# Kernel tuning notes

Hardware: AMD Instinct MI355X
Metric: run time of the kernel (lower is better)

Reference implementation:

```python
import jax, jax.numpy as jnp
import numpy as np

B, N, D, OUT = 4, 4096, 2048, 2048
E, RANK, TOP_K = 8, 16, 2
ALPHA = 16.0
SCALING = ALPHA / RANK


def setup_inputs() -> dict:
    key = jax.random.key(0)
    k1, k2, k3, k4 = jax.random.split(key, 4)
    x = jax.random.normal(k1, (B, N, D), dtype=jnp.float32)
    weight = jax.random.normal(k2, (OUT, D), dtype=jnp.float32) * (1.0 / np.sqrt(D))
    router_w = jax.random.normal(k3, (E, D), dtype=jnp.float32) * 0.02
    experts_A = jax.random.normal(k4, (E, D, RANK), dtype=jnp.float32) * (1.0 / np.sqrt(RANK))
    # experts_B is zero-initialized in the module; use small random values so the
    # LoRA branch contributes non-trivially to the output for kernel testing.
    experts_B = jax.random.normal(jax.random.fold_in(key, 5), (E, RANK, OUT), dtype=jnp.float32) * 0.02
    return {"x": x, "weight": weight, "router_w": router_w,
            "experts_A": experts_A, "experts_B": experts_B}


def reference(x, weight, router_w, experts_A, experts_B):
    # base = F.linear(x, weight)  (no bias)
    base = jnp.einsum('bnd,od->bno', x, weight)
    # router logits: x @ W_r^T -> (B, N, E)
    logits = jnp.einsum('bnd,ed->bne', x, router_w)
    # top-k sparse routing: keep top-k logits, set rest to -inf, softmax
    topk_vals, topk_idx = jax.lax.top_k(logits, TOP_K)  # (B,N,K)
    keep = jax.nn.one_hot(topk_idx, E, dtype=jnp.bool_).any(axis=-2)  # (B,N,E)
    masked = jnp.where(keep, logits, -jnp.inf)
    router_weights = jax.nn.softmax(masked, axis=-1)  # (B,N,E)
    # per-expert low-rank down/up projection, weighted by router
    lora_down = jnp.einsum('bnd,edr->bner', x, experts_A)  # (B,N,E,rank)
    weighted = lora_down * router_weights[..., None]
    moe_out = jnp.einsum('bner,erd->bnd', weighted, experts_B)  # (B,N,OUT)
    return base + SCALING * moe_out
```

## Files before the change

kernel.cpp:

```cpp
#include <hip/hip_runtime.h>
#include <stdint.h>

#define D_DIM 2048
#define OUT_DIM 2048
#define NTOK 16384
#define SCALING 1.0f
#define NT_TILES 34

typedef unsigned short u16;
typedef __attribute__((ext_vector_type(8))) short s16x8;
typedef __attribute__((ext_vector_type(4))) float f32x4;

#define WZ_OFF  0u
#define AZ_OFF  8388608u
#define BZ_OFF  8912896u
#define CZ_OFF  9437184u
#define W8_OFF  13631488u
#define XB_OFF  14155776u
#define WS_BIG   81264640u

__device__ inline u16 f2bf(float f) {
  union { float f; uint32_t u; } v; v.f = f;
  uint32_t u = v.u;
  u += 0x7FFFu + ((u >> 16) & 1u);
  return (u16)(u >> 16);
}

__global__ __launch_bounds__(256) void k_prep(const float* __restrict__ W,
                                              const float* __restrict__ A,
                                              const float* __restrict__ Bf,
                                              u16* __restrict__ Wz,
                                              u16* __restrict__ Az,
                                              u16* __restrict__ Bz) {
  int bid = blockIdx.x;
  if (bid < 4096) {
    int idx = bid * 256 + threadIdx.x;
    int o  = idx >> 9;
    int k0 = (idx & 511) * 4;
    const float4 v = *(const float4*)&W[(size_t)o * D_DIM + k0];
    int s = (o & 7) << 3;
    int dst = (k0 & ~63) | ((k0 & 63) ^ s);
    uint32_t p0 = (uint32_t)f2bf(v.x) | ((uint32_t)f2bf(v.y) << 16);
    uint32_t p1 = (uint32_t)f2bf(v.z) | ((uint32_t)f2bf(v.w) << 16);
    *(uint2*)&Wz[(size_t)o * D_DIM + dst] = make_uint2(p0, p1);
  } else if (bid < 5120) {
    int idx = (bid - 4096) * 256 + threadIdx.x;
    float v = A[idx];
    int r = idx & 15;
    int d = (idx >> 4) & 2047;
    int e = idx >> 15;
    int er = e * 16 + r;
    int s = (er & 7) << 3;
    int dst = (d & ~63) | ((d & 63) ^ s);
    Az[(size_t)er * D_DIM + dst] = f2bf(v);
  } else {
    int idx = (bid - 5120) * 256 + threadIdx.x;
    float v = Bf[idx];
    int er = idx >> 11;
    int o  = idx & 2047;
    int s = (o & 7) << 3;
    int dst = (er & 64) | ((er & 63) ^ s);
    Bz[(size_t)o * 128 + dst] = f2bf(v);
  }
}

__global__ __launch_bounds__(256) void k_router_xb(const float* __restrict__ x,
                                                   const float* __restrict__ rw,
                                                   float* __restrict__ w8,
                                                   u16* __restrict__ xb) {
  int lane = threadIdx.x & 63, wid = threadIdx.x >> 6;
  int t = blockIdx.x * 4 + wid;
  const float* xr = x + (size_t)t * D_DIM;
  float4 xv[8];
#pragma unroll
  for (int j = 0; j < 8; ++j) xv[j] = *(const float4*)&xr[j * 256 + lane * 4];
  int s = (t & 7) << 3;
#pragma unroll
  for (int j = 0; j < 8; ++j) {
    int c4 = j * 256 + lane * 4;
    int dst = (c4 & ~63) | ((c4 & 63) ^ s);
    uint32_t p0 = (uint32_t)f2bf(xv[j].x) | ((uint32_t)f2bf(xv[j].y) << 16);
    uint32_t p1 = (uint32_t)f2bf(xv[j].z) | ((uint32_t)f2bf(xv[j].w) << 16);
    *(uint2*)&xb[(size_t)t * D_DIM + dst] = make_uint2(p0, p1);
  }
  float lg[8];
#pragma unroll
  for (int e = 0; e < 8; ++e) {
    float a = 0.f;
#pragma unroll
    for (int j = 0; j < 8; ++j) {
      float4 rv = *(const float4*)&rw[e * D_DIM + j * 256 + lane * 4];
      a = fmaf(xv[j].x, rv.x, a); a = fmaf(xv[j].y, rv.y, a);
      a = fmaf(xv[j].z, rv.z, a); a = fmaf(xv[j].w, rv.w, a);
    }
#pragma unroll
    for (int off = 32; off; off >>= 1) a += __shfl_xor(a, off, 64);
    lg[e] = a;
  }
  int i0 = 0;
#pragma unroll
  for (int e = 1; e < 8; ++e) if (lg[e] > lg[i0]) i0 = e;
  int i1 = (i0 == 0) ? 1 : 0;
#pragma unroll
  for (int e = 0; e < 8; ++e) if (e != i0 && lg[e] > lg[i1]) i1 = e;
  float e1 = expf(lg[i1] - lg[i0]);
  float inv = 1.f / (1.f + e1);
  float w0 = inv * SCALING, w1 = e1 * inv * SCALING;
  if (lane < 8)
    w8[(size_t)t * 8 + lane] = (lane == i0) ? w0 : (lane == i1) ? w1 : 0.f;
}

__global__ __launch_bounds__(256) void k_lora64(const u16* __restrict__ xb,
                                                const u16* __restrict__ Az,
                                                const float* __restrict__ w8,
                                                u16* __restrict__ Cz) {
  __shared__ u16 Alds[64 * 64];
  __shared__ u16 Blds[128 * 64];
  __shared__ float w8s[64 * 8];
  int tid = threadIdx.x, lane = tid & 63, wid = tid >> 6;
  int t0 = blockIdx.x * 64;
  w8s[tid] = w8[(size_t)t0 * 8 + tid];
  w8s[256 + tid] = w8[(size_t)t0 * 8 + 256 + tid];
  f32x4 acc[8];
#pragma unroll
  for (int n = 0; n < 8; ++n) acc[n] = (f32x4){0.f, 0.f, 0.f, 0.f};
  const int ce = (lane >> 4) * 8;
  for (int kc = 0; kc < 32; ++kc) {
    __syncthreads();
#pragma unroll
    for (int i = 0; i < 2; ++i) {
      const u16* g = xb + (size_t)(t0 + i * 32 + (tid >> 3)) * D_DIM + kc * 64 + (tid & 7) * 8;
      __builtin_amdgcn_global_load_lds(
          (const __attribute__((address_space(1))) void*)g,
          (__attribute__((address_space(3))) void*)(Alds + i * 2048 + tid * 8), 16, 0, 0);
    }
#pragma unroll
    for (int i = 0; i < 4; ++i) {
      const u16* g = Az + (size_t)(i * 32 + (tid >> 3)) * D_DIM + kc * 64 + (tid & 7) * 8;
      __builtin_amdgcn_global_load_lds(
          (const __attribute__((address_space(1))) void*)g,
          (__attribute__((address_space(3))) void*)(Blds + i * 2048 + tid * 8), 16, 0, 0);
    }
    __syncthreads();
#pragma unroll
    for (int kk = 0; kk < 2; ++kk) {
      int ar = wid * 16 + (lane & 15);
      s16x8 af = *(const s16x8*)&Alds[ar * 64 + ((ce + kk * 32) ^ ((ar & 7) << 3))];
#pragma unroll
      for (int nf = 0; nf < 8; ++nf) {
        int br = nf * 16 + (lane & 15);
        s16x8 bf = *(const s16x8*)&Blds[br * 64 + ((ce + kk * 32) ^ ((br & 7) << 3))];
        acc[nf] = __builtin_amdgcn_mfma_f32_16x16x32_bf16(af, bf, acc[nf], 0, 0, 0);
      }
    }
  }
#pragma unroll
  for (int q = 0; q < 4; ++q) {
    int rloc = wid * 16 + (lane >> 4) * 4 + q;
#pragma unroll
    for (int nf = 0; nf < 8; ++nf) {
      int er = nf * 16 + (lane & 15);
      float v = acc[nf][q] * w8s[rloc * 8 + (er >> 4)];
      int dst = (er & 64) | ((er & 63) ^ ((rloc & 7) << 3));
      Cz[(size_t)(t0 + rloc) * 128 + dst] = f2bf(v);
    }
  }
}

__device__ inline void stg(int kt, int h, int t0, int o0,
                           const u16* __restrict__ xb, const u16* __restrict__ Wz,
                           const u16* __restrict__ Cz, const u16* __restrict__ Bz,
                           u16* AshP, u16* BshP, int tid) {
  int p = kt & 1;
  const u16* src; int ld; size_t r0; int c0; u16* dst;
  if (h < 2) {
    if (kt < 32) { src = xb; ld = D_DIM; c0 = kt * 64; }
    else         { src = Cz; ld = 128;   c0 = (kt - 32) * 64; }
    r0 = (size_t)t0 + h * 128;
    dst = AshP + p * 16384 + h * 8192;
  } else {
    if (kt < 32) { src = Wz; ld = D_DIM; c0 = kt * 64; }
    else         { src = Bz; ld = 128;   c0 = (kt - 32) * 64; }
    r0 = (size_t)o0 + (h - 2) * 128;
    dst = BshP + p * 16384 + (h - 2) * 8192;
  }
#pragma unroll
  for (int i = 0; i < 2; ++i) {
    const u16* g = src + (r0 + i * 64 + (tid >> 3)) * (size_t)ld + c0 + (tid & 7) * 8;
    __builtin_amdgcn_global_load_lds(
        (const __attribute__((address_space(1))) void*)g,
        (__attribute__((address_space(3))) void*)(dst + i * 4096 + tid * 8), 16, 0, 0);
  }
}

__device__ inline void read_af(const u16* buf, int rbase, int ce, s16x8 a[4][2]) {
#pragma unroll
  for (int i = 0; i < 4; ++i)
#pragma unroll
    for (int kk = 0; kk < 2; ++kk) {
      int r = rbase + i * 16;
      a[i][kk] = *(const s16x8*)&buf[r * 64 + ((ce + kk * 32) ^ ((r & 7) << 3))];
    }
}

__device__ inline void read_b2(const u16* buf, int rbase, int ce, s16x8 b[4][2], int h) {
#pragma unroll
  for (int i = 0; i < 2; ++i)
#pragma unroll
    for (int kk = 0; kk < 2; ++kk) {
      int r = rbase + (h * 2 + i) * 16;
      b[h * 2 + i][kk] = *(const s16x8*)&buf[r * 64 + ((ce + kk * 32) ^ ((r & 7) << 3))];
    }
}

template <int MFH, int NFH>
__device__ inline void mfma_quad(f32x4 acc[8][4], const s16x8 a[4][2],
                                 const s16x8 b[4][2]) {
#pragma unroll
  for (int i = 0; i < 4; ++i)
#pragma unroll
    for (int j = 0; j < 2; ++j)
#pragma unroll
      for (int kk = 0; kk < 2; ++kk)
        acc[MFH * 4 + i][NFH * 2 + j] = __builtin_amdgcn_mfma_f32_16x16x32_bf16(
            a[i][kk], b[NFH * 2 + j][kk], acc[MFH * 4 + i][NFH * 2 + j], 0, 0, 0);
}

__global__ __launch_bounds__(512, 2) void k_main8(const u16* __restrict__ xb,
                                                  const u16* __restrict__ Wz,
                                                  const u16* __restrict__ Cz,
                                                  const u16* __restrict__ Bz,
                                                  float* __restrict__ out) {
  __shared__ u16 Ash[2][16384];
  __shared__ u16 Bsh[2][16384];
  const int tid = threadIdx.x, lane = tid & 63;
  const int wid = tid >> 6, wm = wid >> 2, wn = wid & 3;
  int bid = blockIdx.x;
  int swz = (bid & 7) * 64 + (bid >> 3);
  int mt = swz >> 3, nt = swz & 7;
  int t0 = mt * 256, o0 = nt * 256;
  const int ce = (lane >> 4) * 8;
  const int arb = wm * 128 + (lane & 15);
  const int brb = wn * 64 + (lane & 15);
  u16* A0 = &Ash[0][0];
  u16* B0 = &Bsh[0][0];

  f32x4 acc[8][4];
#pragma unroll
  for (int m = 0; m < 8; ++m)
#pragma unroll
    for (int n = 0; n < 4; ++n) acc[m][n] = (f32x4){0.f, 0.f, 0.f, 0.f};
  s16x8 a[4][2], b[4][2];

  stg(0, 0, t0, o0, xb, Wz, Cz, Bz, A0, B0, tid);
  stg(0, 1, t0, o0, xb, Wz, Cz, Bz, A0, B0, tid);
  stg(0, 2, t0, o0, xb, Wz, Cz, Bz, A0, B0, tid);
  stg(0, 3, t0, o0, xb, Wz, Cz, Bz, A0, B0, tid);
  stg(1, 0, t0, o0, xb, Wz, Cz, Bz, A0, B0, tid);
  stg(1, 1, t0, o0, xb, Wz, Cz, Bz, A0, B0, tid);
  stg(1, 2, t0, o0, xb, Wz, Cz, Bz, A0, B0, tid);
  stg(1, 3, t0, o0, xb, Wz, Cz, Bz, A0, B0, tid);
  asm volatile("s_waitcnt vmcnt(8)" ::: "memory");
  __builtin_amdgcn_s_barrier();

  for (int kt = 0; kt < NT_TILES; ++kt) {
    const int p = kt & 1;
    const u16* Abuf = &Ash[p][0];
    const u16* Bbuf = &Bsh[p][0];
    const int ktc = (kt + 2 < NT_TILES) ? kt + 2 : NT_TILES - 1;
    read_af(Abuf, arb, ce, a);
    read_b2(Bbuf, brb, ce, b, 0);
    __builtin_amdgcn_s_barrier();
    asm volatile("s_waitcnt lgkmcnt(0)" ::: "memory");
    __builtin_amdgcn_sched_barrier(0);
    __builtin_amdgcn_s_setprio(1);
    mfma_quad<0, 0>(acc, a, b);
    __builtin_amdgcn_s_setprio(0);
    __builtin_amdgcn_s_barrier();
    read_b2(Bbuf, brb, ce, b, 1);
    __builtin_amdgcn_s_barrier();
    asm volatile("s_waitcnt lgkmcnt(0)" ::: "memory");
    __builtin_amdgcn_sched_barrier(0);
    __builtin_amdgcn_s_setprio(1);
    mfma_quad<0, 1>(acc, a, b);
    __builtin_amdgcn_s_setprio(0);
    __builtin_amdgcn_s_barrier();
    read_af(Abuf, arb + 64, ce, a);
    stg(ktc, 2, t0, o0, xb, Wz, Cz, Bz, A0, B0, tid);
    stg(ktc, 3, t0, o0, xb, Wz, Cz, Bz, A0, B0, tid);
    __builtin_amdgcn_s_barrier();
    asm volatile("s_waitcnt lgkmcnt(0)" ::: "memory");
    __builtin_amdgcn_sched_barrier(0);
    __builtin_amdgcn_s_setprio(1);
    mfma_quad<1, 0>(acc, a, b);
    __builtin_amdgcn_s_setprio(0);
    __builtin_amdgcn_s_barrier();
    stg(ktc, 0, t0, o0, xb, Wz, Cz, Bz, A0, B0, tid);
    stg(ktc, 1, t0, o0, xb, Wz, Cz, Bz, A0, B0, tid);
    asm volatile("s_waitcnt vmcnt(8)" ::: "memory");
    __builtin_amdgcn_s_barrier();
    __builtin_amdgcn_s_setprio(1);
    mfma_quad<1, 1>(acc, a, b);
    __builtin_amdgcn_s_setprio(0);
    __builtin_amdgcn_s_barrier();
  }

#pragma unroll
  for (int mf = 0; mf < 8; ++mf)
#pragma unroll
    for (int q = 0; q < 4; ++q) {
      int row = t0 + wm * 128 + mf * 16 + (lane >> 4) * 4 + q;
#pragma unroll
      for (int nf = 0; nf < 4; ++nf) {
        int col = o0 + wn * 64 + nf * 16 + (lane & 15);
        out[(size_t)row * OUT_DIM + col] = acc[mf][nf][q];
      }
    }
}

extern "C" void kernel_launch(void* const* d_in, const int* in_sizes, int n_in,
                              void* d_out, int out_size, void* d_ws, size_t ws_size,
                              hipStream_t stream) {
  const float* x  = (const float*)d_in[0];
  const float* W  = (const float*)d_in[1];
  const float* rw = (const float*)d_in[2];
  const float* eA = (const float*)d_in[3];
  const float* eB = (const float*)d_in[4];
  float* out = (float*)d_out;
  char* ws = (char*)d_ws;
  if (ws_size < WS_BIG) return;

  u16*   Wz = (u16*)(ws + WZ_OFF);
  u16*   Az = (u16*)(ws + AZ_OFF);
  u16*   Bz = (u16*)(ws + BZ_OFF);
  u16*   Cz = (u16*)(ws + CZ_OFF);
  float* w8 = (float*)(ws + W8_OFF);
  u16*   xb = (u16*)(ws + XB_OFF);

  k_prep<<<6144, 256, 0, stream>>>(W, eA, eB, Wz, Az, Bz);
  k_router_xb<<<4096, 256, 0, stream>>>(x, rw, w8, xb);
  k_lora64<<<256, 256, 0, stream>>>(xb, Az, w8, Cz);
  k_main8<<<512, 512, 0, stream>>>(xb, Wz, Cz, Bz, out);
}
```

Measured before the change: 267.1 us.

## Fuse prep and router kernels, double-buffer LoRA loads, restructure main GEMM pipeline

Merges the weight-prep and router/x-conversion kernels into one launch, removing a kernel boundary. The LoRA down-projection kernel gains double-buffered LDS staging, so the next K-chunk loads while MFMAs run on the current one. The main GEMM loop is reorganised so that global-to-LDS stages for tile kt+1/kt+2 and LDS fragment reads for the next tile are issued earlier, with fewer barriers per iteration. This raises LDS use in k_lora64 and makes correctness depend on careful vmcnt/barrier accounting.

```diff
diff --git a/kernel.cpp b/kernel.cpp
--- a/kernel.cpp
+++ b/kernel.cpp
@@ -26,12 +26,12 @@
   return (u16)(u >> 16);
 }
 
-__global__ __launch_bounds__(256) void k_prep(const float* __restrict__ W,
-                                              const float* __restrict__ A,
-                                              const float* __restrict__ Bf,
-                                              u16* __restrict__ Wz,
-                                              u16* __restrict__ Az,
-                                              u16* __restrict__ Bz) {
+__global__ __launch_bounds__(256) void k_prep_router(
+    const float* __restrict__ W, const float* __restrict__ A,
+    const float* __restrict__ Bf, const float* __restrict__ x,
+    const float* __restrict__ rw,
+    u16* __restrict__ Wz, u16* __restrict__ Az, u16* __restrict__ Bz,
+    float* __restrict__ w8, u16* __restrict__ xb) {
   int bid = blockIdx.x;
   if (bid < 4096) {
     int idx = bid * 256 + threadIdx.x;
@@ -43,7 +43,9 @@
     uint32_t p0 = (uint32_t)f2bf(v.x) | ((uint32_t)f2bf(v.y) << 16);
     uint32_t p1 = (uint32_t)f2bf(v.z) | ((uint32_t)f2bf(v.w) << 16);
     *(uint2*)&Wz[(size_t)o * D_DIM + dst] = make_uint2(p0, p1);
-  } else if (bid < 5120) {
+    return;
+  }
+  if (bid < 5120) {
     int idx = (bid - 4096) * 256 + threadIdx.x;
     float v = A[idx];
     int r = idx & 15;
@@ -53,7 +55,9 @@
     int s = (er & 7) << 3;
     int dst = (d & ~63) | ((d & 63) ^ s);
     Az[(size_t)er * D_DIM + dst] = f2bf(v);
-  } else {
+    return;
+  }
+  if (bid < 6144) {
     int idx = (bid - 5120) * 256 + threadIdx.x;
     float v = Bf[idx];
     int er = idx >> 11;
@@ -61,15 +65,10 @@
     int s = (o & 7) << 3;
     int dst = (er & 64) | ((er & 63) ^ s);
     Bz[(size_t)o * 128 + dst] = f2bf(v);
-  }
-}
-
-__global__ __launch_bounds__(256) void k_router_xb(const float* __restrict__ x,
-                                                   const float* __restrict__ rw,
-                                                   float* __restrict__ w8,
-                                                   u16* __restrict__ xb) {
+    return;
+  }
   int lane = threadIdx.x & 63, wid = threadIdx.x >> 6;
-  int t = blockIdx.x * 4 + wid;
+  int t = (bid - 6144) * 4 + wid;
   const float* xr = x + (size_t)t * D_DIM;
   float4 xv[8];
 #pragma unroll
@@ -114,8 +113,8 @@
                                                 const u16* __restrict__ Az,
                                                 const float* __restrict__ w8,
                                                 u16* __restrict__ Cz) {
-  __shared__ u16 Alds[64 * 64];
-  __shared__ u16 Blds[128 * 64];
+  __shared__ u16 Alds[2][64 * 64];
+  __shared__ u16 Blds[2][128 * 64];
   __shared__ float w8s[64 * 8];
   int tid = threadIdx.x, lane = tid & 63, wid = tid >> 6;
   int t0 = blockIdx.x * 64;
@@ -125,34 +124,44 @@
 #pragma unroll
   for (int n = 0; n < 8; ++n) acc[n] = (f32x4){0.f, 0.f, 0.f, 0.f};
   const int ce = (lane >> 4) * 8;
-  for (int kc = 0; kc < 32; ++kc) {
-    __syncthreads();
+
+  auto stage = [&](int kc, int buf) {
+    if (kc > 31) kc = 31;
 #pragma unroll
     for (int i = 0; i < 2; ++i) {
       const u16* g = xb + (size_t)(t0 + i * 32 + (tid >> 3)) * D_DIM + kc * 64 + (tid & 7) * 8;
       __builtin_amdgcn_global_load_lds(
           (const __attribute__((address_space(1))) void*)g,
-          (__attribute__((address_space(3))) void*)(Alds + i * 2048 + tid * 8), 16, 0, 0);
+          (__attribute__((address_space(3))) void*)(&Alds[buf][0] + i * 2048 + tid * 8), 16, 0, 0);
     }
 #pragma unroll
     for (int i = 0; i < 4; ++i) {
       const u16* g = Az + (size_t)(i * 32 + (tid >> 3)) * D_DIM + kc * 64 + (tid & 7) * 8;
       __builtin_amdgcn_global_load_lds(
           (const __attribute__((address_space(1))) void*)g,
-          (__attribute__((address_space(3))) void*)(Blds + i * 2048 + tid * 8), 16, 0, 0);
-    }
-    __syncthreads();
+          (__attribute__((address_space(3))) void*)(&Blds[buf][0] + i * 2048 + tid * 8), 16, 0, 0);
+    }
+  };
+
+  stage(0, 0);
+  asm volatile("s_waitcnt vmcnt(0)" ::: "memory");
+  __builtin_amdgcn_s_barrier();
+  for (int kc = 0; kc < 32; ++kc) {
+    int cur = kc & 1;
+    stage(kc + 1, cur ^ 1);
 #pragma unroll
     for (int kk = 0; kk < 2; ++kk) {
       int ar = wid * 16 + (lane & 15);
-      s16x8 af = *(const s16x8*)&Alds[ar * 64 + ((ce + kk * 32) ^ ((ar & 7) << 3))];
+      s16x8 af = *(const s16x8*)&Alds[cur][ar * 64 + ((ce + kk * 32) ^ ((ar & 7) << 3))];
 #pragma unroll
       for (int nf = 0; nf < 8; ++nf) {
         int br = nf * 16 + (lane & 15);
-        s16x8 bf = *(const s16x8*)&Blds[br * 64 + ((ce + kk * 32) ^ ((br & 7) << 3))];
+        s16x8 bf = *(const s16x8*)&Blds[cur][br * 64 + ((ce + kk * 32) ^ ((br & 7) << 3))];
         acc[nf] = __builtin_amdgcn_mfma_f32_16x16x32_bf16(af, bf, acc[nf], 0, 0, 0);
       }
     }
+    asm volatile("s_waitcnt vmcnt(0)" ::: "memory");
+    __builtin_amdgcn_s_barrier();
   }
 #pragma unroll
   for (int q = 0; q < 4; ++q) {
@@ -171,6 +180,7 @@
                            const u16* __restrict__ xb, const u16* __restrict__ Wz,
                            const u16* __restrict__ Cz, const u16* __restrict__ Bz,
                            u16* AshP, u16* BshP, int tid) {
+  if (kt >= NT_TILES) kt = NT_TILES - 1;
   int p = kt & 1;
   const u16* src; int ld; size_t r0; int c0; u16* dst;
   if (h < 2) {
@@ -259,51 +269,53 @@
   stg(1, 0, t0, o0, xb, Wz, Cz, Bz, A0, B0, tid);
   stg(1, 1, t0, o0, xb, Wz, Cz, Bz, A0, B0, tid);
   stg(1, 2, t0, o0, xb, Wz, Cz, Bz, A0, B0, tid);
-  stg(1, 3, t0, o0, xb, Wz, Cz, Bz, A0, B0, tid);
-  asm volatile("s_waitcnt vmcnt(8)" ::: "memory");
+  asm volatile("s_waitcnt vmcnt(6)" ::: "memory");
   __builtin_amdgcn_s_barrier();
+  __builtin_amdgcn_sched_barrier(0);
+  read_af(&Ash[0][0], arb, ce, a);
+  read_b2(&Bsh[0][0], brb, ce, b, 0);
 
   for (int kt = 0; kt < NT_TILES; ++kt) {
     const int p = kt & 1;
     const u16* Abuf = &Ash[p][0];
     const u16* Bbuf = &Bsh[p][0];
-    const int ktc = (kt + 2 < NT_TILES) ? kt + 2 : NT_TILES - 1;
-    read_af(Abuf, arb, ce, a);
-    read_b2(Bbuf, brb, ce, b, 0);
-    __builtin_amdgcn_s_barrier();
     asm volatile("s_waitcnt lgkmcnt(0)" ::: "memory");
     __builtin_amdgcn_sched_barrier(0);
     __builtin_amdgcn_s_setprio(1);
     mfma_quad<0, 0>(acc, a, b);
     __builtin_amdgcn_s_setprio(0);
-    __builtin_amdgcn_s_barrier();
     read_b2(Bbuf, brb, ce, b, 1);
-    __builtin_amdgcn_s_barrier();
+    stg(kt + 1, 3, t0, o0, xb, Wz, Cz, Bz, A0, B0, tid);
+    __builtin_amdgcn_s_barrier();
+    __builtin_amdgcn_sched_barrier(0);
     asm volatile("s_waitcnt lgkmcnt(0)" ::: "memory");
     __builtin_amdgcn_sched_barrier(0);
     __builtin_amdgcn_s_setprio(1);
     mfma_quad<0, 1>(acc, a, b);
     __builtin_amdgcn_s_setprio(0);
-    __builtin_amdgcn_s_barrier();
     read_af(Abuf, arb + 64, ce, a);
-    stg(ktc, 2, t0, o0, xb, Wz, Cz, Bz, A0, B0, tid);
-    stg(ktc, 3, t0, o0, xb, Wz, Cz, Bz, A0, B0, tid);
-    __builtin_amdgcn_s_barrier();
+    __builtin_amdgcn_s_barrier();
+    __builtin_amdgcn_sched_barrier(0);
     asm volatile("s_waitcnt lgkmcnt(0)" ::: "memory");
     __builtin_amdgcn_sched_barrier(0);
     __builtin_amdgcn_s_setprio(1);
     mfma_quad<1, 0>(acc, a, b);
     __builtin_amdgcn_s_setprio(0);
-    __builtin_amdgcn_s_barrier();
-    stg(ktc, 0, t0, o0, xb, Wz, Cz, Bz, A0, B0, tid);
-    stg(ktc, 1, t0, o0, xb, Wz, Cz, Bz, A0, B0, tid);
-    asm volatile("s_waitcnt vmcnt(8)" ::: "memory");
-    __builtin_amdgcn_s_barrier();
+    stg(kt + 2, 0, t0, o0, xb, Wz, Cz, Bz, A0, B0, tid);
+    stg(kt + 2, 1, t0, o0, xb, Wz, Cz, Bz, A0, B0, tid);
+    stg(kt + 2, 2, t0, o0, xb, Wz, Cz, Bz, A0, B0, tid);
+    asm volatile("s_waitcnt vmcnt(6)" ::: "memory");
+    __builtin_amdgcn_s_barrier();
+    __builtin_amdgcn_sched_barrier(0);
     __builtin_amdgcn_s_setprio(1);
     mfma_quad<1, 1>(acc, a, b);
     __builtin_amdgcn_s_setprio(0);
-    __builtin_amdgcn_s_barrier();
-  }
+    read_af(&Ash[p ^ 1][0], arb, ce, a);
+    read_b2(&Bsh[p ^ 1][0], brb, ce, b, 0);
+    __builtin_amdgcn_s_barrier();
+    __builtin_amdgcn_sched_barrier(0);
+  }
+  asm volatile("s_waitcnt vmcnt(0) lgkmcnt(0)" ::: "memory");
 
 #pragma unroll
   for (int mf = 0; mf < 8; ++mf)
@@ -337,8 +349,7 @@
   float* w8 = (float*)(ws + W8_OFF);
   u16*   xb = (u16*)(ws + XB_OFF);
 
-  k_prep<<<6144, 256, 0, stream>>>(W, eA, eB, Wz, Az, Bz);
-  k_router_xb<<<4096, 256, 0, stream>>>(x, rw, w8, xb);
+  k_prep_router<<<10240, 256, 0, stream>>>(W, eA, eB, x, rw, Wz, Az, Bz, w8, xb);
   k_lora64<<<256, 256, 0, stream>>>(xb, Az, w8, Cz);
   k_main8<<<512, 512, 0, stream>>>(xb, Wz, Cz, Bz, out);
 }
```

After: 250.8 us. 1.06x faster.
